# Optimization experiments

Measured on AMD Instinct MI355X. Metric: run time of the kernel, lower is better.

Reference implementation:

```python
import jax, jax.numpy as jnp
import numpy as np

B, SX, SY, D, H = 4, 4096, 4096, 1024, 64


def setup_inputs() -> dict:
    key = jax.random.key(0)
    ks = jax.random.split(key, 7)
    x = jax.random.normal(ks[0], (B, SX, D), dtype=jnp.float32)
    y = jax.random.normal(ks[1], (B, SY, D), dtype=jnp.float32)
    valid_lens_x = jax.random.randint(ks[2], (B,), 1, SX + 1).astype(jnp.int64)
    valid_lens_y = jax.random.randint(ks[3], (B,), 1, SY + 1).astype(jnp.int64)
    s = 1.0 / np.sqrt(D)
    Wq = jax.random.uniform(ks[4], (D, H), jnp.float32, -s, s)
    Wk = jax.random.uniform(ks[5], (D, H), jnp.float32, -s, s)
    Wv = jax.random.uniform(ks[6], (D, H), jnp.float32, -s, s)
    return {"x": x, "y": y, "valid_lens_x": valid_lens_x,
            "valid_lens_y": valid_lens_y, "use_causal": 1,
            "Wq": Wq, "Wk": Wk, "Wv": Wv}


def reference(x, y, valid_lens_x, valid_lens_y, use_causal, Wq, Wk, Wv):
    # projections (Linear, no bias)
    k = x @ Wk                      # [B, Sx, H]
    q = y @ Wq                      # [B, Sy, H]
    v = x @ Wv                      # [B, Sx, H]
    scale = k.shape[-1] ** -0.5
    wei = jnp.einsum('bqh,bkh->bqk', q, k) * scale   # [B, Sy, Sx]
    Sq, Sk = q.shape[1], k.shape[1]
    if use_causal:  # static python int -> tril masked_fill branch
        tril = jnp.tril(jnp.ones((Sq, Sk), dtype=bool))
        wei = jnp.where(tril[None], wei, -jnp.inf)
    # per-sample valid-length cross mask
    kmask = jnp.arange(Sk)[None, :] < valid_lens_x[:, None]   # [B, Sk]
    qmask = jnp.arange(Sq)[None, :] < valid_lens_y[:, None]   # [B, Sq]
    mask = qmask[:, :, None] & kmask[:, None, :]              # [B, Sq, Sk]
    wei = jnp.where(mask, wei, -jnp.inf)
    # NaN-safe softmax: zero out fully-masked rows
    row_mask = jnp.all(jnp.isinf(wei), axis=2, keepdims=True)  # [B, Sq, 1]
    safe = jnp.where(row_mask, 0.0, wei)
    probs = jax.nn.softmax(safe, axis=2)
    probs = jnp.where(row_mask, 0.0, probs)
    # dropout p=0.0 -> identity (eval)
    out = probs @ v                 # [B, Sy, H]
    return out
```

## Files before the change

kernel.cpp:

```cpp
#include <hip/hip_runtime.h>
#include <hip/hip_bf16.h>
#include <stdint.h>

#define BBATCH 4
#define SXN 4096
#define SYN 4096
#define DD 1024
#define HH 64

typedef float f32x4 __attribute__((ext_vector_type(4)));
typedef short bf16x8 __attribute__((ext_vector_type(8)));

static __device__ __forceinline__ unsigned short f2bf(float f) {
  unsigned int u = __float_as_uint(f);
  u += 0x7fffu + ((u >> 16) & 1u);
  return (unsigned short)(u >> 16);
}
static __device__ __forceinline__ float bf2f(unsigned short b) {
  return __uint_as_float(((unsigned int)b) << 16);
}

static __device__ __forceinline__ bf16x8 cvt8(f32x4 lo, f32x4 hi) {
  bf16x8 v;
  v[0] = (short)f2bf(lo[0]); v[1] = (short)f2bf(lo[1]);
  v[2] = (short)f2bf(lo[2]); v[3] = (short)f2bf(lo[3]);
  v[4] = (short)f2bf(hi[0]); v[5] = (short)f2bf(hi[1]);
  v[6] = (short)f2bf(hi[2]); v[7] = (short)f2bf(hi[3]);
  return v;
}

static __device__ __forceinline__ void gload_lds16(const void* g, void* l) {
  __builtin_amdgcn_global_load_lds(
      (const __attribute__((address_space(1))) unsigned int*)g,
      (__attribute__((address_space(3))) unsigned int*)l, 16, 0, 0);
}

__global__ __launch_bounds__(256) void prep_wt(
    const float* __restrict__ Wq, const float* __restrict__ Wk,
    const float* __restrict__ Wv, unsigned short* __restrict__ Wt) {
  int gid = blockIdx.x * 256 + threadIdx.x;
  int mat = gid >> 16;
  int k = gid & 1023;
  int h = (gid >> 10) & 63;
  const float* W = (mat == 0) ? Wk : (mat == 1) ? Wv : Wq;
  Wt[gid] = f2bf(W[k * HH + h]);
}

__global__ __launch_bounds__(256, 3) void proj_kernel(
    const float* __restrict__ xin, const float* __restrict__ yin,
    const unsigned short* __restrict__ Wt,
    unsigned short* __restrict__ Qb, unsigned short* __restrict__ Kb,
    unsigned short* __restrict__ Vt) {
  __shared__ __align__(16) float xa[2][64 * 64];
  const int tid = threadIdx.x;
  const int w = tid >> 6, l = tid & 63;
  const int li = l & 15, lg = l >> 4;
  const bool qpath = blockIdx.x >= 256;
  const int row0 = (qpath ? (blockIdx.x - 256) : (int)blockIdx.x) * 64;
  const float* src = qpath ? yin : xin;
  const unsigned short* WtA = qpath ? (Wt + 2 * 65536) : Wt;
  const unsigned short* WtB = Wt + 65536;

  f32x4 acc0[4], acc1[4];
  const f32x4 z4 = {0.f, 0.f, 0.f, 0.f};
#pragma unroll
  for (int i = 0; i < 4; ++i) { acc0[i] = z4; acc1[i] = z4; }

  auto stage = [&](int bsel, int kc) {
#pragma unroll
    for (int i = 0; i < 4; ++i) {
      const int r = i * 16 + w * 4 + (l >> 4);
      const int c16 = (l & 15) ^ (r & 7);
      const float* g = src + (size_t)(row0 + r) * DD + kc * 64 + c16 * 4;
      float* lp = &xa[bsel][i * 1024 + w * 256];
      gload_lds16(g, lp);
    }
  };

  int buf = 0;
  stage(0, 0);
  __syncthreads();
  for (int kc = 0; kc < 16; ++kc) {
    if (kc < 15) stage(buf ^ 1, kc + 1);
    const int rrow = w * 16 + li;
    const int swz = (rrow & 7) * 4;
#pragma unroll
    for (int ks = 0; ks < 2; ++ks) {
      const int base = rrow * 64 + ks * 32 + lg * 8;
      const f32x4 lo = *reinterpret_cast<const f32x4*>(&xa[buf][base ^ swz]);
      const f32x4 hi = *reinterpret_cast<const f32x4*>(&xa[buf][(base + 4) ^ swz]);
      const bf16x8 a = cvt8(lo, hi);
      const int gks = kc * 2 + ks;
#pragma unroll
      for (int hb = 0; hb < 4; ++hb) {
        const bf16x8 b0 = *reinterpret_cast<const bf16x8*>(
            &WtA[(hb * 16 + li) * 1024 + gks * 32 + lg * 8]);
        acc0[hb] = __builtin_amdgcn_mfma_f32_16x16x32_bf16(a, b0, acc0[hb], 0, 0, 0);
      }
      if (!qpath) {
#pragma unroll
        for (int hb = 0; hb < 4; ++hb) {
          const bf16x8 b1 = *reinterpret_cast<const bf16x8*>(
              &WtB[(hb * 16 + li) * 1024 + gks * 32 + lg * 8]);
          acc1[hb] = __builtin_amdgcn_mfma_f32_16x16x32_bf16(a, b1, acc1[hb], 0, 0, 0);
        }
      }
    }
    __syncthreads();
    buf ^= 1;
  }

  const int rbase = row0 + w * 16 + lg * 4;
  if (qpath) {
#pragma unroll
    for (int hb = 0; hb < 4; ++hb)
#pragma unroll
      for (int r = 0; r < 4; ++r)
        Qb[(size_t)(rbase + r) * HH + hb * 16 + li] = f2bf(acc0[hb][r] * 0.125f);
  } else {
#pragma unroll
    for (int hb = 0; hb < 4; ++hb)
#pragma unroll
      for (int r = 0; r < 4; ++r)
        Kb[(size_t)(rbase + r) * HH + hb * 16 + li] = f2bf(acc0[hb][r]);
    const int b = rbase >> 12;
    const int sx = rbase & 4095;
#pragma unroll
    for (int hb = 0; hb < 4; ++hb) {
      ushort4 o;
      o.x = f2bf(acc1[hb][0]); o.y = f2bf(acc1[hb][1]);
      o.z = f2bf(acc1[hb][2]); o.w = f2bf(acc1[hb][3]);
      *reinterpret_cast<ushort4*>(
          &Vt[((size_t)b * HH + hb * 16 + li) * SXN + sx]) = o;
    }
  }
}

__global__ __launch_bounds__(512, 4) void flash_kernel(
    const unsigned short* __restrict__ Qb, const unsigned short* __restrict__ Kb,
    const unsigned short* __restrict__ Vt, const int* __restrict__ vlx_p,
    const int* __restrict__ vly_p, const int* __restrict__ uc_p,
    float* __restrict__ out) {
  __shared__ __align__(16) unsigned short Pl[8][16][72];
  __shared__ __align__(16) float Ol[8][16][64];
  __shared__ float Ml[8][16], Ll[8][16];

  const int tid = threadIdx.x;
  const int w = tid >> 6, l = tid & 63;
  const int li = l & 15, lg = l >> 4;
  const int rg = w & 1, c = w >> 1;

  const int kblk = blockIdx.x;
  const int b = (kblk & 7) >> 1;
  const int rb = 127 - (((kblk >> 3) << 1) | (kblk & 1));
  const int q0 = rb * 32;
  const int vlx = vlx_p[b], vly = vly_p[b];
  const int causal = uc_p[0];
  const float LOG2E = 1.4426950408889634f;

  const int qbase = q0 + rg * 16;
  int kend = causal ? min(vlx, qbase + 16) : vlx;
  if (kend > SXN) kend = SXN;
  const int nst = (kend + 63) >> 6;
  const int s0 = (c * nst) >> 2;
  const int s1 = ((c + 1) * nst) >> 2;

  const unsigned short* KbB = Kb + (size_t)b * SXN * HH;
  const unsigned short* VtB = Vt + (size_t)b * HH * SXN;

  f32x4 o[4];
  float mrun[4], lrun[4];
  const f32x4 z4 = {0.f, 0.f, 0.f, 0.f};
#pragma unroll
  for (int i = 0; i < 4; ++i) { o[i] = z4; mrun[i] = -INFINITY; lrun[i] = 0.f; }

  const bool active = (qbase < vly);
  const int qg0 = qbase + lg * 4;

  if (active && s1 > s0) {
    const unsigned short* Qrow = Qb + ((size_t)b * SYN + qbase + li) * HH;
    const bf16x8 qa0 = *reinterpret_cast<const bf16x8*>(&Qrow[lg * 8]);
    const bf16x8 qa1 = *reinterpret_cast<const bf16x8*>(&Qrow[32 + lg * 8]);

    for (int s = s0; s < s1; ++s) {
      const int key0 = s << 6;
      f32x4 sa[4];
#pragma unroll
      for (int kb = 0; kb < 4; ++kb) {
        const unsigned short* Kr = &KbB[(size_t)(key0 + kb * 16 + li) * HH];
        const bf16x8 k0 = *reinterpret_cast<const bf16x8*>(&Kr[lg * 8]);
        const bf16x8 k1 = *reinterpret_cast<const bf16x8*>(&Kr[32 + lg * 8]);
        f32x4 acc = z4;
        acc = __builtin_amdgcn_mfma_f32_16x16x32_bf16(qa0, k0, acc, 0, 0, 0);
        acc = __builtin_amdgcn_mfma_f32_16x16x32_bf16(qa1, k1, acc, 0, 0, 0);
        sa[kb] = acc;
      }

#pragma unroll
      for (int r = 0; r < 4; ++r) {
        const int qcap = causal ? (qg0 + r) : 0x7fffffff;
        float sv[4];
#pragma unroll
        for (int kb = 0; kb < 4; ++kb) {
          const int kg = key0 + kb * 16 + li;
          const bool valid = (kg < vlx) && (kg <= qcap);
          sv[kb] = valid ? sa[kb][r] : -1e30f;
        }
        float tm = fmaxf(fmaxf(sv[0], sv[1]), fmaxf(sv[2], sv[3]));
        tm = fmaxf(tm, __shfl_xor(tm, 1));
        tm = fmaxf(tm, __shfl_xor(tm, 2));
        tm = fmaxf(tm, __shfl_xor(tm, 4));
        tm = fmaxf(tm, __shfl_xor(tm, 8));
        const float mn = fmaxf(mrun[r], tm);
        const float corr = exp2f((mrun[r] - mn) * LOG2E);
        mrun[r] = mn;
        float ps = 0.f;
#pragma unroll
        for (int kb = 0; kb < 4; ++kb) {
          const float p = exp2f((sv[kb] - mn) * LOG2E);
          const unsigned short pb = f2bf(p);
          Pl[w][lg * 4 + r][kb * 16 + li] = pb;
          ps += bf2f(pb);
        }
        ps += __shfl_xor(ps, 1);
        ps += __shfl_xor(ps, 2);
        ps += __shfl_xor(ps, 4);
        ps += __shfl_xor(ps, 8);
        lrun[r] = lrun[r] * corr + ps;
#pragma unroll
        for (int df = 0; df < 4; ++df) o[df][r] *= corr;
      }

#pragma unroll
      for (int kh = 0; kh < 2; ++kh) {
        const bf16x8 pa =
            *reinterpret_cast<const bf16x8*>(&Pl[w][li][kh * 32 + lg * 8]);
#pragma unroll
        for (int df = 0; df < 4; ++df) {
          const bf16x8 vb = *reinterpret_cast<const bf16x8*>(
              &VtB[(size_t)(df * 16 + li) * SXN + key0 + kh * 32 + lg * 8]);
          o[df] = __builtin_amdgcn_mfma_f32_16x16x32_bf16(pa, vb, o[df], 0, 0, 0);
        }
      }
    }
  }

  if (active) {
#pragma unroll
    for (int df = 0; df < 4; ++df)
#pragma unroll
      for (int r = 0; r < 4; ++r)
        Ol[w][lg * 4 + r][df * 16 + li] = o[df][r];
    if (li == 0) {
#pragma unroll
      for (int r = 0; r < 4; ++r) {
        Ml[w][lg * 4 + r] = mrun[r];
        Ll[w][lg * 4 + r] = lrun[r];
      }
    }
  }
  __syncthreads();

  {
    float* outB = out + (size_t)b * SYN * HH;
#pragma unroll
    for (int i = 0; i < 4; ++i) {
      const int rr = w * 4 + i;
      const int mrg = rr >> 4;
      const int rowIdx = rr & 15;
      const int q = q0 + rr;
      float res = 0.f;
      if (q < vly) {
        float M = -INFINITY;
#pragma unroll
        for (int cc = 0; cc < 4; ++cc)
          M = fmaxf(M, Ml[(cc << 1) | mrg][rowIdx]);
        if (M > -1e37f) {
          float lsum = 0.f, acc = 0.f;
#pragma unroll
          for (int cc = 0; cc < 4; ++cc) {
            const int ww = (cc << 1) | mrg;
            const float wt = exp2f((Ml[ww][rowIdx] - M) * LOG2E);
            lsum += wt * Ll[ww][rowIdx];
            acc += wt * Ol[ww][rowIdx][l];
          }
          res = (lsum > 0.f) ? acc / lsum : 0.f;
        }
      }
      outB[(size_t)q * HH + l] = res;
    }
  }
}

extern "C" void kernel_launch(void* const* d_in, const int* in_sizes, int n_in,
                              void* d_out, int out_size, void* d_ws, size_t ws_size,
                              hipStream_t stream) {
  const float* x = (const float*)d_in[0];
  const float* y = (const float*)d_in[1];
  const int* vlx = (const int*)d_in[2];
  const int* vly = (const int*)d_in[3];
  const int* uc = (const int*)d_in[4];
  const float* Wq = (const float*)d_in[5];
  const float* Wk = (const float*)d_in[6];
  const float* Wv = (const float*)d_in[7];
  float* out = (float*)d_out;

  char* ws = (char*)d_ws;
  unsigned short* Qb = (unsigned short*)(ws);
  unsigned short* Kb = (unsigned short*)(ws + (2u << 20));
  unsigned short* Vt = (unsigned short*)(ws + (4u << 20));
  unsigned short* Wt = (unsigned short*)(ws + (6u << 20));

  prep_wt<<<768, 256, 0, stream>>>(Wq, Wk, Wv, Wt);
  proj_kernel<<<512, 256, 0, stream>>>(x, y, Wt, Qb, Kb, Vt);
  flash_kernel<<<512, 512, 0, stream>>>(Qb, Kb, Vt, vlx, vly, uc, out);
}
```

Measured before the change: 268.0 us.

## Split flash attention into 16-row blocks with 8-way key split and prefetching

The flash kernel now gives each block 16 query rows instead of 32, launches twice as many blocks, and splits the key range across all 8 waves rather than 4 per row group. Blocks whose rows all lie past the valid query length write zeros and exit early. K and V fragments are loaded into registers before the softmax so global load latency overlaps with the math, and the P and O shared buffers share a union to reduce LDS use. The projection kernel batches its weight loads ahead of the MFMAs and raises its occupancy hint. The changes trade more partial-result merging and register pressure for better load balance and latency hiding.

```diff
diff --git a/kernel.cpp b/kernel.cpp
--- a/kernel.cpp
+++ b/kernel.cpp
@@ -46,7 +46,7 @@
   Wt[gid] = f2bf(W[k * HH + h]);
 }
 
-__global__ __launch_bounds__(256, 3) void proj_kernel(
+__global__ __launch_bounds__(256, 4) void proj_kernel(
     const float* __restrict__ xin, const float* __restrict__ yin,
     const unsigned short* __restrict__ Wt,
     unsigned short* __restrict__ Qb, unsigned short* __restrict__ Kb,
@@ -91,19 +91,24 @@
       const f32x4 hi = *reinterpret_cast<const f32x4*>(&xa[buf][(base + 4) ^ swz]);
       const bf16x8 a = cvt8(lo, hi);
       const int gks = kc * 2 + ks;
-#pragma unroll
-      for (int hb = 0; hb < 4; ++hb) {
-        const bf16x8 b0 = *reinterpret_cast<const bf16x8*>(
+      bf16x8 bA[4], bB[4];
+#pragma unroll
+      for (int hb = 0; hb < 4; ++hb)
+        bA[hb] = *reinterpret_cast<const bf16x8*>(
             &WtA[(hb * 16 + li) * 1024 + gks * 32 + lg * 8]);
-        acc0[hb] = __builtin_amdgcn_mfma_f32_16x16x32_bf16(a, b0, acc0[hb], 0, 0, 0);
-      }
       if (!qpath) {
 #pragma unroll
-        for (int hb = 0; hb < 4; ++hb) {
-          const bf16x8 b1 = *reinterpret_cast<const bf16x8*>(
+        for (int hb = 0; hb < 4; ++hb)
+          bB[hb] = *reinterpret_cast<const bf16x8*>(
               &WtB[(hb * 16 + li) * 1024 + gks * 32 + lg * 8]);
-          acc1[hb] = __builtin_amdgcn_mfma_f32_16x16x32_bf16(a, b1, acc1[hb], 0, 0, 0);
-        }
+      }
+#pragma unroll
+      for (int hb = 0; hb < 4; ++hb)
+        acc0[hb] = __builtin_amdgcn_mfma_f32_16x16x32_bf16(a, bA[hb], acc0[hb], 0, 0, 0);
+      if (!qpath) {
+#pragma unroll
+        for (int hb = 0; hb < 4; ++hb)
+          acc1[hb] = __builtin_amdgcn_mfma_f32_16x16x32_bf16(a, bB[hb], acc1[hb], 0, 0, 0);
       }
     }
     __syncthreads();
@@ -136,34 +141,44 @@
   }
 }
 
+union FlashSm {
+  unsigned short Pl[8][16][72];
+  float Ol[8][16][64];
+};
+
 __global__ __launch_bounds__(512, 4) void flash_kernel(
     const unsigned short* __restrict__ Qb, const unsigned short* __restrict__ Kb,
     const unsigned short* __restrict__ Vt, const int* __restrict__ vlx_p,
     const int* __restrict__ vly_p, const int* __restrict__ uc_p,
     float* __restrict__ out) {
-  __shared__ __align__(16) unsigned short Pl[8][16][72];
-  __shared__ __align__(16) float Ol[8][16][64];
+  __shared__ __align__(16) FlashSm sm;
   __shared__ float Ml[8][16], Ll[8][16];
 
   const int tid = threadIdx.x;
   const int w = tid >> 6, l = tid & 63;
   const int li = l & 15, lg = l >> 4;
-  const int rg = w & 1, c = w >> 1;
 
   const int kblk = blockIdx.x;
   const int b = (kblk & 7) >> 1;
-  const int rb = 127 - (((kblk >> 3) << 1) | (kblk & 1));
-  const int q0 = rb * 32;
+  const int g = 255 - (((kblk >> 3) << 1) | (kblk & 1));
+  const int q0 = g * 16;
   const int vlx = vlx_p[b], vly = vly_p[b];
   const int causal = uc_p[0];
   const float LOG2E = 1.4426950408889634f;
 
-  const int qbase = q0 + rg * 16;
-  int kend = causal ? min(vlx, qbase + 16) : vlx;
+  float* outB = out + (size_t)b * SYN * HH;
+
+  if (q0 >= vly) {
+    *reinterpret_cast<float2*>(&outB[(size_t)q0 * HH + tid * 2]) =
+        make_float2(0.f, 0.f);
+    return;
+  }
+
+  int kend = causal ? min(vlx, q0 + 16) : vlx;
   if (kend > SXN) kend = SXN;
   const int nst = (kend + 63) >> 6;
-  const int s0 = (c * nst) >> 2;
-  const int s1 = ((c + 1) * nst) >> 2;
+  const int s0 = (w * nst) >> 3;
+  const int s1 = ((w + 1) * nst) >> 3;
 
   const unsigned short* KbB = Kb + (size_t)b * SXN * HH;
   const unsigned short* VtB = Vt + (size_t)b * HH * SXN;
@@ -174,27 +189,36 @@
 #pragma unroll
   for (int i = 0; i < 4; ++i) { o[i] = z4; mrun[i] = -INFINITY; lrun[i] = 0.f; }
 
-  const bool active = (qbase < vly);
-  const int qg0 = qbase + lg * 4;
-
-  if (active && s1 > s0) {
-    const unsigned short* Qrow = Qb + ((size_t)b * SYN + qbase + li) * HH;
+  const int qg0 = q0 + lg * 4;
+
+  if (s1 > s0) {
+    const unsigned short* Qrow = Qb + ((size_t)b * SYN + q0 + li) * HH;
     const bf16x8 qa0 = *reinterpret_cast<const bf16x8*>(&Qrow[lg * 8]);
     const bf16x8 qa1 = *reinterpret_cast<const bf16x8*>(&Qrow[32 + lg * 8]);
 
     for (int s = s0; s < s1; ++s) {
       const int key0 = s << 6;
-      f32x4 sa[4];
+      bf16x8 f[8];
 #pragma unroll
       for (int kb = 0; kb < 4; ++kb) {
         const unsigned short* Kr = &KbB[(size_t)(key0 + kb * 16 + li) * HH];
-        const bf16x8 k0 = *reinterpret_cast<const bf16x8*>(&Kr[lg * 8]);
-        const bf16x8 k1 = *reinterpret_cast<const bf16x8*>(&Kr[32 + lg * 8]);
+        f[kb * 2] = *reinterpret_cast<const bf16x8*>(&Kr[lg * 8]);
+        f[kb * 2 + 1] = *reinterpret_cast<const bf16x8*>(&Kr[32 + lg * 8]);
+      }
+      f32x4 sa[4];
+#pragma unroll
+      for (int kb = 0; kb < 4; ++kb) {
         f32x4 acc = z4;
-        acc = __builtin_amdgcn_mfma_f32_16x16x32_bf16(qa0, k0, acc, 0, 0, 0);
-        acc = __builtin_amdgcn_mfma_f32_16x16x32_bf16(qa1, k1, acc, 0, 0, 0);
+        acc = __builtin_amdgcn_mfma_f32_16x16x32_bf16(qa0, f[kb * 2], acc, 0, 0, 0);
+        acc = __builtin_amdgcn_mfma_f32_16x16x32_bf16(qa1, f[kb * 2 + 1], acc, 0, 0, 0);
         sa[kb] = acc;
       }
+#pragma unroll
+      for (int kh = 0; kh < 2; ++kh)
+#pragma unroll
+        for (int df = 0; df < 4; ++df)
+          f[kh * 4 + df] = *reinterpret_cast<const bf16x8*>(
+              &VtB[(size_t)(df * 16 + li) * SXN + key0 + kh * 32 + lg * 8]);
 
 #pragma unroll
       for (int r = 0; r < 4; ++r) {
@@ -219,7 +243,7 @@
         for (int kb = 0; kb < 4; ++kb) {
           const float p = exp2f((sv[kb] - mn) * LOG2E);
           const unsigned short pb = f2bf(p);
-          Pl[w][lg * 4 + r][kb * 16 + li] = pb;
+          sm.Pl[w][lg * 4 + r][kb * 16 + li] = pb;
           ps += bf2f(pb);
         }
         ps += __shfl_xor(ps, 1);
@@ -234,55 +258,48 @@
 #pragma unroll
       for (int kh = 0; kh < 2; ++kh) {
         const bf16x8 pa =
-            *reinterpret_cast<const bf16x8*>(&Pl[w][li][kh * 32 + lg * 8]);
-#pragma unroll
-        for (int df = 0; df < 4; ++df) {
-          const bf16x8 vb = *reinterpret_cast<const bf16x8*>(
-              &VtB[(size_t)(df * 16 + li) * SXN + key0 + kh * 32 + lg * 8]);
-          o[df] = __builtin_amdgcn_mfma_f32_16x16x32_bf16(pa, vb, o[df], 0, 0, 0);
-        }
-      }
-    }
-  }
-
-  if (active) {
-#pragma unroll
-    for (int df = 0; df < 4; ++df)
-#pragma unroll
-      for (int r = 0; r < 4; ++r)
-        Ol[w][lg * 4 + r][df * 16 + li] = o[df][r];
-    if (li == 0) {
-#pragma unroll
-      for (int r = 0; r < 4; ++r) {
-        Ml[w][lg * 4 + r] = mrun[r];
-        Ll[w][lg * 4 + r] = lrun[r];
-      }
-    }
-  }
+            *reinterpret_cast<const bf16x8*>(&sm.Pl[w][li][kh * 32 + lg * 8]);
+#pragma unroll
+        for (int df = 0; df < 4; ++df)
+          o[df] = __builtin_amdgcn_mfma_f32_16x16x32_bf16(pa, f[kh * 4 + df],
+                                                          o[df], 0, 0, 0);
+      }
+    }
+  }
+
   __syncthreads();
 
+#pragma unroll
+  for (int df = 0; df < 4; ++df)
+#pragma unroll
+    for (int r = 0; r < 4; ++r)
+      sm.Ol[w][lg * 4 + r][df * 16 + li] = o[df][r];
+  if (li == 0) {
+#pragma unroll
+    for (int r = 0; r < 4; ++r) {
+      Ml[w][lg * 4 + r] = mrun[r];
+      Ll[w][lg * 4 + r] = lrun[r];
+    }
+  }
+  __syncthreads();
+
   {
-    float* outB = out + (size_t)b * SYN * HH;
-#pragma unroll
-    for (int i = 0; i < 4; ++i) {
-      const int rr = w * 4 + i;
-      const int mrg = rr >> 4;
-      const int rowIdx = rr & 15;
+#pragma unroll
+    for (int i = 0; i < 2; ++i) {
+      const int rr = w * 2 + i;
       const int q = q0 + rr;
       float res = 0.f;
       if (q < vly) {
         float M = -INFINITY;
 #pragma unroll
-        for (int cc = 0; cc < 4; ++cc)
-          M = fmaxf(M, Ml[(cc << 1) | mrg][rowIdx]);
+        for (int cc = 0; cc < 8; ++cc) M = fmaxf(M, Ml[cc][rr]);
         if (M > -1e37f) {
           float lsum = 0.f, acc = 0.f;
 #pragma unroll
-          for (int cc = 0; cc < 4; ++cc) {
-            const int ww = (cc << 1) | mrg;
-            const float wt = exp2f((Ml[ww][rowIdx] - M) * LOG2E);
-            lsum += wt * Ll[ww][rowIdx];
-            acc += wt * Ol[ww][rowIdx][l];
+          for (int cc = 0; cc < 8; ++cc) {
+            const float wt = exp2f((Ml[cc][rr] - M) * LOG2E);
+            lsum += wt * Ll[cc][rr];
+            acc += wt * sm.Ol[cc][rr][l];
           }
           res = (lsum > 0.f) ? acc / lsum : 0.f;
         }
@@ -313,5 +330,5 @@
 
   prep_wt<<<768, 256, 0, stream>>>(Wq, Wk, Wv, Wt);
   proj_kernel<<<512, 256, 0, stream>>>(x, y, Wt, Qb, Kb, Vt);
-  flash_kernel<<<512, 512, 0, stream>>>(Qb, Kb, Vt, vlx, vly, uc, out);
-}
+  flash_kernel<<<1024, 512, 0, stream>>>(Qb, Kb, Vt, vlx, vly, uc, out);
+}
```

Measured after the change: 250.2 us. -6.7%, faster.
